# Optimization experiments

Hardware: AMD Instinct MI355X
Metric: run time of the kernel (lower is better)

Reference implementation:

```python
import jax, jax.numpy as jnp
import numpy as np

B = 4096          # fused tokens (batch)
E = 1024          # attnConfig embed_size == MoE emb_size
OUT = E // 4      # per-branch feature dim (self.output)
N_EXP = 8         # number of experts
TOP = 2           # top-k routing
H = 8             # attention heads
HD = E // H       # head dim
HID = 4 * E       # expert MLP hidden
IMG = 64 * 64     # flattened single-channel image
W_IMP = 0.01      # importance loss weight


def setup_inputs() -> dict:
    key = jax.random.key(0)
    ks = jax.random.split(key, 24)
    n = lambda i, shp, sc=1.0: jax.random.normal(ks[i], shp, jnp.float32) * sc
    inp = {
        'source': n(0, (B, 1, 64, 64)),
        'target': n(1, (B, 1, 64, 64)),
        'background': n(2, (B, 1, 64, 64)),
        'image': n(3, (B, E)),
        'text': n(4, (B, E)),
        # shared encoder (stub: flatten -> fc to OUT, shared across s/t/b)
        'W_enc': n(5, (IMG, OUT), 0.02), 'b_enc': jnp.zeros((OUT,), jnp.float32),
        # linerImg
        'W_img': n(6, (E, OUT), 0.02), 'b_img': jnp.zeros((OUT,), jnp.float32),
        # cross attention
        'Wq': n(7, (E, E), 0.02), 'bq': jnp.zeros((E,), jnp.float32),
        'Wk': n(8, (E, E), 0.02), 'bk': jnp.zeros((E,), jnp.float32),
        'Wv': n(9, (E, E), 0.02), 'bv': jnp.zeros((E,), jnp.float32),
        'Wo': n(10, (E, E), 0.02), 'bo': jnp.zeros((E,), jnp.float32),
        # gate
        'W_gate': n(11, (E, N_EXP), 0.02), 'b_gate': jnp.zeros((N_EXP,), jnp.float32),
        # experts: per-expert 2-layer MLP E->HID->E
        'W1': n(12, (N_EXP, E, HID), 0.02), 'b1': jnp.zeros((N_EXP, HID), jnp.float32),
        'W2': n(13, (N_EXP, HID, E), 0.02), 'b2': jnp.zeros((N_EXP, E), jnp.float32),
    }
    return inp


def reference(source, target, background, image, text,
              W_enc, b_enc, W_img, b_img,
              Wq, bq, Wk, bk, Wv, bv, Wo, bo,
              W_gate, b_gate, W1, b1, W2, b2):
    enc = lambda a: a.reshape(a.shape[0], -1) @ W_enc + b_enc      # shared_encoder stub
    s = enc(source); t = enc(target); bg = enc(background)        # [B, OUT] each
    img = jax.nn.silu(image @ W_img + b_img)                      # [B, OUT]
    x = jnp.concatenate([s, t, bg, img], axis=1)                  # [B, E] visionFeatures

    # cross attention with seq_len 1 for both x (query) and text (key/value)
    q = (x @ Wq + bq).reshape(B, H, HD)
    k = (text @ Wk + bk).reshape(B, H, HD)
    v = (text @ Wv + bv).reshape(B, H, HD)
    scores = jnp.sum(q * k, axis=-1, keepdims=True) / jnp.sqrt(jnp.float32(HD))  # [B,H,1]
    attw = jax.nn.softmax(scores[..., None], axis=-1)[..., 0]     # softmax over 1 key == 1
    att = (attw * v).reshape(B, E) @ Wo + bo                       # [B, E]

    gate_logits = att @ W_gate + b_gate                            # [B, N_EXP]
    gate_prob = jax.nn.softmax(gate_logits, axis=-1)               # eval mode: no noise
    top_w, top_idx = jax.lax.top_k(gate_prob, TOP)                 # [B, TOP]
    top_w = jax.nn.softmax(top_w, axis=-1)                         # renormalize over top-k

    # dense-dispatch equivalent of the per-expert gather/index_add loop
    h = jax.nn.gelu(jnp.einsum('be,neh->nbh', x, W1) + b1[:, None, :])   # [N,B,HID]
    y_all = jnp.einsum('nbh,nhe->nbe', h, W2) + b2[:, None, :]           # [N,B,E]
    combine = jnp.zeros((B, N_EXP), jnp.float32).at[
        jnp.arange(B)[:, None], top_idx].add(top_w)                      # [B,N]
    y = jnp.einsum('nbe,bn->be', y_all, combine)                          # [B,E]

    importance = gate_prob.sum(axis=0)                             # [N_EXP]
    importance_loss = W_IMP * (jnp.std(importance, ddof=1) / jnp.mean(importance)) ** 2
    return (y, gate_prob, importance_loss)
```

## Files before the change

kernel.cpp:

```cpp
#include <hip/hip_runtime.h>
#include <hip/hip_bf16.h>
#include <stdint.h>

typedef __bf16 bf16_t;
typedef bf16_t bf16x8 __attribute__((ext_vector_type(8)));
typedef float f32x4 __attribute__((ext_vector_type(4)));
typedef uint16_t u16x8 __attribute__((ext_vector_type(8)));

static constexpr int B_TOK  = 4096;
static constexpr int E_DIM  = 1024;
static constexpr int N_EXPC = 8;
static constexpr int HID    = 4096;
static constexpr int IMGSZ  = 4096;
static constexpr int NSLOT  = 2 * B_TOK;
static constexpr int NTIL   = 71;

#define DEVI __device__ __forceinline__

DEVI int imin(int a, int b) { return a < b ? a : b; }

DEVI uint16_t f2bf(float f) {
  union { float f; uint32_t u; } v; v.f = f;
  uint32_t u = v.u;
  return (uint16_t)((u + 0x7FFFu + ((u >> 16) & 1u)) >> 16);
}

DEVI void gload_lds16(const void* g, void* l) {
  __builtin_amdgcn_global_load_lds((const __attribute__((address_space(1))) void*)g,
                                   (__attribute__((address_space(3))) void*)l, 16, 0, 0);
}

template<int N> DEVI void waitv() {
  if constexpr (N == 0)       asm volatile("s_waitcnt vmcnt(0)" ::: "memory");
  else if constexpr (N == 4)  asm volatile("s_waitcnt vmcnt(4)" ::: "memory");
  else if constexpr (N == 8)  asm volatile("s_waitcnt vmcnt(8)" ::: "memory");
  else if constexpr (N == 10) asm volatile("s_waitcnt vmcnt(10)" ::: "memory");
}

#define BAR() do { __builtin_amdgcn_sched_barrier(0); __builtin_amdgcn_s_barrier(); \
                   __builtin_amdgcn_sched_barrier(0); } while (0)

#define MFMA16(a, b, c) __builtin_amdgcn_mfma_f32_16x16x32_bf16((a), (b), (c), 0, 0, 0)

DEVI void transW_body(int bid, const float* W1, const float* W2,
                      const float* We, const float* Wi,
                      uint16_t* W1T, uint16_t* W2T, uint16_t* WeT, uint16_t* WiT,
                      float (*tile)[65])
{
  const float* in; uint16_t* out; int R, C, c0, r0;
  if (bid < 8192) {
    int e = bid >> 10, rem = bid & 1023;
    R = 1024; C = 4096;
    c0 = (rem & 63) * 64; r0 = (rem >> 6) * 64;
    in = W1 + (size_t)e * R * C; out = W1T + (size_t)e * R * C;
  } else if (bid < 16384) {
    int i = bid - 8192; int e = i >> 10, rem = i & 1023;
    R = 4096; C = 1024;
    c0 = (rem & 15) * 64; r0 = (rem >> 4) * 64;
    in = W2 + (size_t)e * R * C; out = W2T + (size_t)e * R * C;
  } else if (bid < 16640) {
    int i = bid - 16384;
    R = 4096; C = 256;
    c0 = (i & 3) * 64; r0 = (i >> 2) * 64;
    in = We; out = WeT;
  } else {
    int i = bid - 16640;
    R = 1024; C = 256;
    c0 = (i & 3) * 64; r0 = (i >> 2) * 64;
    in = Wi; out = WiT;
  }
  int t = threadIdx.x;
  #pragma unroll
  for (int i = 0; i < 4; ++i) {
    int rr = i * 16 + (t >> 4), c4 = (t & 15) * 4;
    f32x4 v = *(const f32x4*)&in[(size_t)(r0 + rr) * C + c0 + c4];
    tile[rr][c4 + 0] = v[0]; tile[rr][c4 + 1] = v[1];
    tile[rr][c4 + 2] = v[2]; tile[rr][c4 + 3] = v[3];
  }
  __syncthreads();
  #pragma unroll
  for (int i = 0; i < 2; ++i) {
    int c = i * 32 + (t >> 3), j = t & 7;
    u16x8 o;
    #pragma unroll
    for (int k = 0; k < 8; ++k) o[k] = f2bf(tile[j * 8 + k][c]);
    *(u16x8*)&out[(size_t)(c0 + c) * R + r0 + j * 8] = o;
  }
}

DEVI void matf_body(int kblk, const float* W, const float* G, float* out)
{
  int k = kblk * 4 + (threadIdx.x >> 6);
  int lane = threadIdx.x & 63;
  float a0 = 0.f, a1 = 0.f, a2 = 0.f, a3 = 0.f, a4 = 0.f, a5 = 0.f, a6 = 0.f, a7 = 0.f;
  for (int m = lane; m < E_DIM; m += 64) {
    float w = W[(size_t)k * E_DIM + m];
    const float* gm = &G[m * 8];
    a0 = __builtin_fmaf(w, gm[0], a0); a1 = __builtin_fmaf(w, gm[1], a1);
    a2 = __builtin_fmaf(w, gm[2], a2); a3 = __builtin_fmaf(w, gm[3], a3);
    a4 = __builtin_fmaf(w, gm[4], a4); a5 = __builtin_fmaf(w, gm[5], a5);
    a6 = __builtin_fmaf(w, gm[6], a6); a7 = __builtin_fmaf(w, gm[7], a7);
  }
  #pragma unroll
  for (int off = 32; off; off >>= 1) {
    a0 += __shfl_xor(a0, off); a1 += __shfl_xor(a1, off);
    a2 += __shfl_xor(a2, off); a3 += __shfl_xor(a3, off);
    a4 += __shfl_xor(a4, off); a5 += __shfl_xor(a5, off);
    a6 += __shfl_xor(a6, off); a7 += __shfl_xor(a7, off);
  }
  if (lane == 0) {
    float* o = &out[k * 8];
    o[0] = a0; o[1] = a1; o[2] = a2; o[3] = a3;
    o[4] = a4; o[5] = a5; o[6] = a6; o[7] = a7;
  }
}

__global__ __launch_bounds__(256)
void prep1_k(const float* __restrict__ W1, const float* __restrict__ W2,
             const float* __restrict__ We, const float* __restrict__ Wi,
             uint16_t* __restrict__ W1T, uint16_t* __restrict__ W2T,
             uint16_t* __restrict__ WeT, uint16_t* __restrict__ WiT,
             const float* __restrict__ Wo, const float* __restrict__ Wg,
             float* __restrict__ g1c,
             const float* __restrict__ bv, float* __restrict__ part,
             int* __restrict__ counts)
{
  __shared__ float tile[64][65];
  int bid = blockIdx.x;
  if (bid < 16704) {
    transW_body(bid, W1, W2, We, Wi, W1T, W2T, WeT, WiT, tile);
  } else if (bid < 16960) {
    matf_body(bid - 16704, Wo, Wg, g1c);
  } else if (bid < 16968) {
    int b = bid - 16960, t = threadIdx.x;
    f32x4 acc = {0.f, 0.f, 0.f, 0.f};
    for (int k = b * 128; k < b * 128 + 128; ++k) {
      float s = bv[k];
      f32x4 w = *(const f32x4*)&Wo[(size_t)k * E_DIM + t * 4];
      acc[0] = __builtin_fmaf(s, w[0], acc[0]);
      acc[1] = __builtin_fmaf(s, w[1], acc[1]);
      acc[2] = __builtin_fmaf(s, w[2], acc[2]);
      acc[3] = __builtin_fmaf(s, w[3], acc[3]);
    }
    *(f32x4*)&part[(size_t)b * E_DIM + t * 4] = acc;
  } else {
    if (threadIdx.x < 8) counts[threadIdx.x] = 0;
  }
}

__global__ __launch_bounds__(256)
void prep2_k(const float* __restrict__ Wv, const float* __restrict__ g1c,
             float* __restrict__ G3,
             const float* __restrict__ part, const float* __restrict__ bo,
             const float* __restrict__ Wg, const float* __restrict__ bg,
             float* __restrict__ gb)
{
  int bid = blockIdx.x;
  if (bid < 256) {
    matf_body(bid, Wv, g1c, G3);
  } else {
    __shared__ float t1s[E_DIM];
    int t = threadIdx.x;
    for (int j = t; j < E_DIM; j += 256) {
      float s = bo[j];
      #pragma unroll
      for (int b = 0; b < 8; ++b) s += part[(size_t)b * E_DIM + j];
      t1s[j] = s;
    }
    __syncthreads();
    int wave = t >> 6, lane = t & 63;
    #pragma unroll
    for (int ei = 0; ei < 2; ++ei) {
      int e = wave * 2 + ei;
      float s = 0.f;
      for (int m = lane; m < E_DIM; m += 64) s = __builtin_fmaf(t1s[m], Wg[m * 8 + e], s);
      #pragma unroll
      for (int off = 32; off; off >>= 1) s += __shfl_xor(s, off);
      if (lane == 0) gb[e] = s + bg[e];
    }
  }
}

__global__ __launch_bounds__(256)
void gate_k(const float* __restrict__ text, const float* __restrict__ G3,
            const float* __restrict__ gb, float* __restrict__ gate_out,
            int* __restrict__ topIdx, float* __restrict__ topW,
            int* __restrict__ counts)
{
  __shared__ __align__(16) float sT[E_DIM];
  __shared__ float lg[8];
  int b = blockIdx.x, t = threadIdx.x;
  *(f32x4*)&sT[t * 4] = *(const f32x4*)&text[(size_t)b * E_DIM + t * 4];
  __syncthreads();
  int wave = t >> 6, lane = t & 63;
  #pragma unroll
  for (int ei = 0; ei < 2; ++ei) {
    int e = wave * 2 + ei;
    float s = 0.f;
    for (int k = lane; k < E_DIM; k += 64) s = __builtin_fmaf(sT[k], G3[k * 8 + e], s);
    #pragma unroll
    for (int off = 32; off; off >>= 1) s += __shfl_down(s, off);
    if (lane == 0) lg[e] = s + gb[e];
  }
  __syncthreads();
  if (t == 0) {
    float p[8];
    float mx = lg[0];
    for (int i = 1; i < 8; i++) mx = fmaxf(mx, lg[i]);
    float den = 0.f;
    for (int i = 0; i < 8; i++) { p[i] = __expf(lg[i] - mx); den += p[i]; }
    float inv = 1.f / den;
    for (int i = 0; i < 8; i++) { p[i] *= inv; gate_out[(size_t)b * 8 + i] = p[i]; }
    int i1 = 0;
    for (int i = 1; i < 8; i++) if (p[i] > p[i1]) i1 = i;
    int i2 = (i1 == 0) ? 1 : 0;
    for (int i = 0; i < 8; i++) if (i != i1 && p[i] > p[i2]) i2 = i;
    float ex = __expf(p[i2] - p[i1]);
    float w1 = 1.f / (1.f + ex), w2 = ex / (1.f + ex);
    topIdx[b * 2] = i1; topIdx[b * 2 + 1] = i2;
    topW[b * 2] = w1;  topW[b * 2 + 1] = w2;
    atomicAdd(&counts[i1], 1);
    atomicAdd(&counts[i2], 1);
  }
}

__global__ __launch_bounds__(256)
void post_k(const float* __restrict__ gate_out, float* __restrict__ out_loss,
            const int* __restrict__ counts, const int* __restrict__ topIdx,
            const float* __restrict__ topW,
            int* __restrict__ meta, int* __restrict__ perm,
            int* __restrict__ slotOf)
{
  int t = threadIdx.x;
  if (blockIdx.x == 0) {
    float s[8] = {0.f, 0.f, 0.f, 0.f, 0.f, 0.f, 0.f, 0.f};
    for (int b = t; b < B_TOK; b += 256) {
      const float* g = &gate_out[(size_t)b * 8];
      #pragma unroll
      for (int e = 0; e < 8; ++e) s[e] += g[e];
    }
    __shared__ float red[8][256];
    #pragma unroll
    for (int e = 0; e < 8; ++e) red[e][t] = s[e];
    __syncthreads();
    for (int off = 128; off; off >>= 1) {
      if (t < off)
        #pragma unroll
        for (int e = 0; e < 8; ++e) red[e][t] += red[e][t + off];
      __syncthreads();
    }
    if (t == 0) {
      float m = 0.f;
      for (int e = 0; e < 8; e++) m += red[e][0];
      m *= 0.125f;
      float v = 0.f;
      for (int e = 0; e < 8; e++) { float d = red[e][0] - m; v += d * d; }
      v /= 7.f;
      out_loss[0] = 0.01f * v / (m * m);
    }
  } else {
    __shared__ int sBases[8];
    __shared__ int sCursor[8];
    if (t == 0) {
      int a = 0, nt = 0;
      for (int e = 0; e < 8; e++) {
        sBases[e] = a; sCursor[e] = 0;
        int c = counts[e];
        for (int j = 0; j < c; j += 128) {
          meta[1 + 3 * nt] = e;
          meta[2 + 3 * nt] = a + j;
          meta[3 + 3 * nt] = (c - j < 128) ? (c - j) : 128;
          nt++;
        }
        a += c;
      }
      meta[0] = nt;
    }
    __syncthreads();
    for (int b = t; b < B_TOK; b += 256) {
      #pragma unroll
      for (int j = 0; j < 2; j++) {
        int e = topIdx[b * 2 + j];
        int pos = atomicAdd(&sCursor[e], 1);
        int slot = sBases[e] + pos;
        perm[slot] = b;
        slotOf[b * 2 + j] = slot;
      }
    }
  }
}

template<int BN, int EPI, bool GATHER, int NT>
__global__ __launch_bounds__(256, 3)
void gemm_p(const uint16_t* __restrict__ Ab, int lda,
            const uint16_t* __restrict__ BT, void* __restrict__ Cv, int ldc,
            const float* __restrict__ bias, int K,
            const int* __restrict__ meta, const int* __restrict__ perm,
            size_t bStride, int biasStride)
{
  constexpr int HN = BN / 2, FN = BN / 32;
  constexpr int OPS = (BN == 128 ? 4 : 3);
  constexpr int TOTAL = NTIL * NT, Q = TOTAL / 8, FULLB = 64 * NT;
  int bid = blockIdx.x;
  int wg = (bid & 7) * Q + (bid >> 3);
  int mtile, nt;
  if (wg < FULLB) { int rem = wg % (8 * NT); mtile = (wg / (8 * NT)) * 8 + (rem & 7); nt = rem >> 3; }
  else            { int rem = wg - FULLB;    mtile = 64 + rem % 7;                    nt = rem / 7; }
  if (mtile >= meta[0]) return;
  int e = meta[1 + 3 * mtile], rowBase = meta[2 + 3 * mtile], rows = meta[3 + 3 * mtile];
  const uint16_t* Bt = BT + (size_t)e * bStride;
  const float* bi = bias + (size_t)e * (size_t)biasStride;

  constexpr int ABUF = 8192;
  constexpr int BBUF = (BN == 128) ? 8192 : 4096;
  __shared__ __align__(16) char sAraw[3 * ABUF];
  __shared__ __align__(16) char sBraw[3 * BBUF];

  int t = threadIdx.x, wave = t >> 6, lane = t & 63;
  int wr = wave >> 1, wc = wave & 1;

  int rB = t >> 2;
  int slB = ((t & 3) ^ (rB & 3)) * 8;
  const uint16_t* gB0 = Bt + (size_t)(nt * BN + rB) * K + slB;
  const uint16_t* gB1 = Bt + (size_t)(nt * BN + rB + 64) * K + slB;

  int r0 = t >> 2, r1 = r0 + 64;
  int sl = ((t & 3) ^ (r0 & 3)) * 8;
  int rr0 = imin(r0, rows - 1), rr1 = imin(r1, rows - 1);
  int car0 = GATHER ? perm[rowBase + rr0] : rowBase + rr0;
  int car1 = GATHER ? perm[rowBase + rr1] : rowBase + rr1;
  const uint16_t* gA0 = Ab + (size_t)car0 * lda + sl;
  const uint16_t* gA1 = Ab + (size_t)car1 * lda + sl;

  char* laW = sAraw + wave * 1024;
  char* lbW = sBraw + wave * 1024;
  auto STAGE = [&](int kt, int c) {
    int ko = kt << 5;
    char* la = laW + c * ABUF;
    char* lb = lbW + c * BBUF;
    gload_lds16(gA0 + ko, la);
    gload_lds16(gA1 + ko, la + 4096);
    gload_lds16(gB0 + ko, lb);
    if constexpr (BN == 128) gload_lds16(gB1 + ko, lb + 4096);
  };

  f32x4 acc[4][FN];
  #pragma unroll
  for (int m = 0; m < 4; m++)
    #pragma unroll
    for (int n = 0; n < FN; n++)
      acc[m][n] = f32x4{0.f, 0.f, 0.f, 0.f};

  STAGE(0, 0);
  STAGE(1, 1);

  int fr = lane & 15;
  int rdoff = ((lane >> 4) ^ (lane & 3)) * 16;
  int c0 = 0, c2 = 2;
  int nk = K >> 5;

  for (int kt = 0; kt < nk; ++kt) {
    if (kt + 2 < nk) { STAGE(kt + 2, c2); waitv<2 * OPS>(); }
    else if (kt + 1 < nk) waitv<OPS>();
    else waitv<0>();
    BAR();

    const char* bA = sAraw + c0 * ABUF;
    const char* bB = sBraw + c0 * BBUF;
    bf16x8 af[4], bfr[FN];
    #pragma unroll
    for (int m = 0; m < 4; m++)
      af[m] = *(const bf16x8*)(bA + (wr * 64 + m * 16 + fr) * 64 + rdoff);
    #pragma unroll
    for (int n = 0; n < FN; n++)
      bfr[n] = *(const bf16x8*)(bB + (wc * HN + n * 16 + fr) * 64 + rdoff);
    #pragma unroll
    for (int m = 0; m < 4; m++)
      #pragma unroll
      for (int n = 0; n < FN; n++)
        acc[m][n] = MFMA16(af[m], bfr[n], acc[m][n]);

    BAR();
    c0 = (c0 == 2) ? 0 : c0 + 1;
    c2 = (c2 == 2) ? 0 : c2 + 1;
  }

  #pragma unroll
  for (int m = 0; m < 4; m++) {
    int lrow = wr * 64 + m * 16 + (lane >> 4) * 4;
    #pragma unroll
    for (int n = 0; n < FN; n++) {
      int col = nt * BN + wc * HN + n * 16 + (lane & 15);
      float bval = bi[col];
      #pragma unroll
      for (int r = 0; r < 4; r++) {
        int lr = lrow + r;
        if (lr >= rows) continue;
        float v = acc[m][n][r] + bval;
        size_t cr = (size_t)(rowBase + lr) * ldc + col;
        if (EPI == 3) {
          float u = v + 0.044715f * v * v * v;
          v = v / (1.f + __expf(-1.5957691216057308f * u));
          ((uint16_t*)Cv)[cr] = f2bf(v);
        } else {
          ((float*)Cv)[cr] = v;
        }
      }
    }
  }
}

__global__ __launch_bounds__(256, 3)
void gemm_encR(const float* __restrict__ F0, const float* __restrict__ F1,
               const float* __restrict__ F2, const float* __restrict__ Fimg,
               const uint16_t* __restrict__ BTe, const uint16_t* __restrict__ BTi,
               float* __restrict__ Penc, float* __restrict__ Pimg)
{
  int z = blockIdx.z;
  const float* Af; const uint16_t* BT; float* P; int K, kc;
  if (z < 12) {
    int br = z / 4; kc = z % 4;
    Af = (br == 0) ? F0 : (br == 1) ? F1 : F2;
    BT = BTe; P = Penc + (size_t)z * B_TOK * 256; K = IMGSZ;
  } else {
    kc = z - 12;
    Af = Fimg; BT = BTi; P = Pimg + (size_t)kc * B_TOK * 256; K = E_DIM;
  }
  int Kc = (z < 12) ? (K / 4) : (K / 2);
  int k0 = kc * Kc;
  int rowBase = blockIdx.x * 64, nt = blockIdx.y;

  __shared__ __align__(16) char sB[3 * 8192];
  int t = threadIdx.x, wave = t >> 6, lane = t & 63;
  int fr = lane & 15, q4 = lane >> 4;

  const float* gA = Af + (size_t)(rowBase + wave * 16 + fr) * K + k0 + q4 * 8;

  int rloc = t >> 2;
  int ssw = ((t & 3) ^ (rloc & 3)) * 8;
  const uint16_t* gB0 = BT + (size_t)(nt * 128 + rloc) * K + k0 + ssw;
  const uint16_t* gB1 = gB0 + (size_t)64 * K;

  auto STB = [&](int kt, int c) {
    gload_lds16(gB0 + kt * 32, sB + c * 8192 + wave * 1024);
    gload_lds16(gB1 + kt * 32, sB + c * 8192 + 4096 + wave * 1024);
  };

  f32x4 acc[8];
  #pragma unroll
  for (int n = 0; n < 8; ++n) acc[n] = f32x4{0.f, 0.f, 0.f, 0.f};

  int nk = Kc >> 5;
  STB(0, 0); STB(1, 1);
  f32x4 aE0 = *(const f32x4*)(gA),      aE1 = *(const f32x4*)(gA + 4);
  f32x4 aO0 = *(const f32x4*)(gA + 32), aO1 = *(const f32x4*)(gA + 36);
  int c0 = 0, c2 = 2;
  int bRow = (q4 ^ (fr & 3)) * 16;

  auto step = [&](int kt, f32x4& aX0, f32x4& aX1) {
    bool m2 = kt + 2 < nk;
    if (m2) STB(kt + 2, c2);
    bf16x8 a;
    a[0] = (bf16_t)aX0[0]; a[1] = (bf16_t)aX0[1]; a[2] = (bf16_t)aX0[2]; a[3] = (bf16_t)aX0[3];
    a[4] = (bf16_t)aX1[0]; a[5] = (bf16_t)aX1[1]; a[6] = (bf16_t)aX1[2]; a[7] = (bf16_t)aX1[3];
    int kp = m2 ? kt + 2 : kt;
    aX0 = *(const f32x4*)(gA + kp * 32);
    aX1 = *(const f32x4*)(gA + kp * 32 + 4);
    if (m2) waitv<10>(); else waitv<0>();
    BAR();
    const char* bb = sB + c0 * 8192;
    bf16x8 bfr[8];
    #pragma unroll
    for (int n = 0; n < 8; ++n)
      bfr[n] = *(const bf16x8*)(bb + n * 1024 + fr * 64 + bRow);
    #pragma unroll
    for (int n = 0; n < 8; ++n) acc[n] = MFMA16(a, bfr[n], acc[n]);
    BAR();
    c0 = (c0 == 2) ? 0 : c0 + 1;
    c2 = (c2 == 2) ? 0 : c2 + 1;
  };

  for (int kt = 0; kt < nk; kt += 2) {
    step(kt, aE0, aE1);
    step(kt + 1, aO0, aO1);
  }

  #pragma unroll
  for (int n = 0; n < 8; ++n) {
    int col = nt * 128 + n * 16 + fr;
    #pragma unroll
    for (int r = 0; r < 4; ++r) {
      int row = rowBase + wave * 16 + q4 * 4 + r;
      P[(size_t)row * 256 + col] = acc[n][r];
    }
  }
}

__global__ __launch_bounds__(256)
void redu_k(const float* __restrict__ Penc, const float* __restrict__ Pimg,
            const float* __restrict__ bEnc, const float* __restrict__ bImg,
            uint16_t* __restrict__ xb)
{
  int y = blockIdx.y;
  int row = blockIdx.x * 4 + (threadIdx.x >> 6);
  int c4 = (threadIdx.x & 63) * 4;
  bool img = (y == 3);
  const float* bias = img ? bImg : bEnc;
  f32x4 s = *(const f32x4*)&bias[c4];
  const float* p = (img ? Pimg : Penc + (size_t)y * 4 * B_TOK * 256)
                   + (size_t)row * 256 + c4;
  int SK = img ? 2 : 4;
  for (int kc = 0; kc < SK; ++kc)
    s += *(const f32x4*)(p + (size_t)kc * B_TOK * 256);
  if (img) {
    #pragma unroll
    for (int j = 0; j < 4; ++j) s[j] = s[j] / (1.f + __expf(-s[j]));
  }
  ushort4 o;
  o.x = f2bf(s[0]); o.y = f2bf(s[1]); o.z = f2bf(s[2]); o.w = f2bf(s[3]);
  *(ushort4*)&xb[(size_t)row * E_DIM + y * 256 + c4] = o;
}

__global__ __launch_bounds__(256)
void combine_k(const float* __restrict__ Yg, const int* __restrict__ slotOf,
               const float* __restrict__ topW, float* __restrict__ y)
{
  int b = blockIdx.x, t = threadIdx.x;
  int s0 = slotOf[b * 2], s1 = slotOf[b * 2 + 1];
  float w0 = topW[b * 2], w1 = topW[b * 2 + 1];
  f32x4 a = *(const f32x4*)&Yg[(size_t)s0 * E_DIM + t * 4];
  f32x4 c = *(const f32x4*)&Yg[(size_t)s1 * E_DIM + t * 4];
  f32x4 r = a * w0 + c * w1;
  *(f32x4*)&y[(size_t)b * E_DIM + t * 4] = r;
}

extern "C" void kernel_launch(void* const* d_in, const int* in_sizes, int n_in,
                              void* d_out, int out_size, void* d_ws, size_t ws_size,
                              hipStream_t stream)
{
  (void)in_sizes; (void)n_in; (void)out_size;
  const float* src   = (const float*)d_in[0];
  const float* tgt   = (const float*)d_in[1];
  const float* bgr   = (const float*)d_in[2];
  const float* image = (const float*)d_in[3];
  const float* text  = (const float*)d_in[4];
  const float* W_enc = (const float*)d_in[5];
  const float* b_enc = (const float*)d_in[6];
  const float* W_img = (const float*)d_in[7];
  const float* b_img = (const float*)d_in[8];
  const float* Wv    = (const float*)d_in[13];
  const float* bv    = (const float*)d_in[14];
  const float* Wo    = (const float*)d_in[15];
  const float* bo    = (const float*)d_in[16];
  const float* Wg    = (const float*)d_in[17];
  const float* bgg   = (const float*)d_in[18];
  const float* W1    = (const float*)d_in[19];
  const float* b1    = (const float*)d_in[20];
  const float* W2    = (const float*)d_in[21];
  const float* b2    = (const float*)d_in[22];

  float* out_y    = (float*)d_out;
  float* out_gate = out_y + (size_t)B_TOK * E_DIM;
  float* out_loss = out_gate + (size_t)B_TOK * N_EXPC;

  char* p = (char*)d_ws;
  auto alloc = [&](size_t bytes) { char* r = p; p += (bytes + 255) & ~(size_t)255; return r; };
  uint16_t* WencT = (uint16_t*)alloc((size_t)256 * IMGSZ * 2);
  uint16_t* WimgT = (uint16_t*)alloc((size_t)256 * E_DIM * 2);
  uint16_t* W1T   = (uint16_t*)alloc((size_t)N_EXPC * HID * E_DIM * 2);
  uint16_t* W2T   = (uint16_t*)alloc((size_t)N_EXPC * E_DIM * HID * 2);
  float* part  = (float*)alloc((size_t)8 * E_DIM * 4);
  float* g1c   = (float*)alloc((size_t)E_DIM * 8 * 4);
  float* G3    = (float*)alloc((size_t)E_DIM * 8 * 4);
  float* gbv   = (float*)alloc(64 * 4);
  int*   topIdx = (int*)alloc(B_TOK * 2 * 4);
  float* topW   = (float*)alloc(B_TOK * 2 * 4);
  int*   slotOf = (int*)alloc(B_TOK * 2 * 4);
  int*   counts = (int*)alloc(64 * 4);
  int*   meta   = (int*)alloc((1 + 3 * (NTIL + 1)) * 4 + 64);
  int*   perm   = (int*)alloc(NSLOT * 4);
  uint16_t* xbf  = (uint16_t*)alloc((size_t)B_TOK * E_DIM * 2);
  uint16_t* Hbuf = (uint16_t*)alloc((size_t)NSLOT * HID * 2);
  char* uni = alloc((size_t)14 * B_TOK * 256 * 4);
  float* Penc = (float*)uni;
  float* Pimg = Penc + (size_t)12 * B_TOK * 256;
  float* Yg   = (float*)uni;
  if ((size_t)(p - (char*)d_ws) > ws_size) return;

  prep1_k<<<dim3(16969), 256, 0, stream>>>(W1, W2, W_enc, W_img, W1T, W2T, WencT, WimgT,
                                           Wo, Wg, g1c, bv, part, counts);
  prep2_k<<<dim3(257), 256, 0, stream>>>(Wv, g1c, G3, part, bo, Wg, bgg, gbv);
  gate_k<<<B_TOK, 256, 0, stream>>>(text, G3, gbv, out_gate, topIdx, topW, counts);
  post_k<<<dim3(2), 256, 0, stream>>>(out_gate, out_loss, counts, topIdx, topW,
                                      meta, perm, slotOf);
  gemm_encR<<<dim3(B_TOK / 64, 2, 14), 256, 0, stream>>>(
      src, tgt, bgr, image, WencT, WimgT, Penc, Pimg);
  redu_k<<<dim3(B_TOK / 4, 4), 256, 0, stream>>>(Penc, Pimg, b_enc, b_img, xbf);

  gemm_p<128, 3, true, HID / 128><<<dim3(NTIL * (HID / 128)), 256, 0, stream>>>(
      xbf, E_DIM, W1T, Hbuf, HID, b1, E_DIM, meta, perm, (size_t)HID * E_DIM, HID);
  gemm_p<128, 0, false, E_DIM / 128><<<dim3(NTIL * (E_DIM / 128)), 256, 0, stream>>>(
      Hbuf, HID, W2T, Yg, E_DIM, b2, HID, meta, perm, (size_t)E_DIM * HID, E_DIM);

  combine_k<<<B_TOK, 256, 0, stream>>>(Yg, slotOf, topW, out_y);
}
```

Before: 636.6 us.

## Halve encoder split-K, fuse routing into reduction kernel, store expert output in bf16

The encoder GEMM now splits K in two instead of four (the image branch is not split at all), which halves the partial-sum buffers written and read by the reduction. The routing/post kernel is merged into the reduction kernel as extra blocks, removing one launch. The second expert GEMM writes bf16 instead of fp32, and the combine kernel converts it back, cutting the traffic for the expert output. The trade-offs are fewer encoder blocks, hence less parallelism, and an extra bf16 rounding of the expert outputs before they are combined.

```diff
diff --git a/kernel.cpp b/kernel.cpp
--- a/kernel.cpp
+++ b/kernel.cpp
@@ -23,6 +23,10 @@
   union { float f; uint32_t u; } v; v.f = f;
   uint32_t u = v.u;
   return (uint16_t)((u + 0x7FFFu + ((u >> 16) & 1u)) >> 16);
+}
+
+DEVI float bf2f(uint16_t u) {
+  union { uint32_t i; float f; } v; v.i = (uint32_t)u << 16; return v.f;
 }
 
 DEVI void gload_lds16(const void* g, void* l) {
@@ -224,14 +228,244 @@
   }
 }
 
+template<int BN, int EPI, bool GATHER, int NT>
+__global__ __launch_bounds__(256, 3)
+void gemm_p(const uint16_t* __restrict__ Ab, int lda,
+            const uint16_t* __restrict__ BT, void* __restrict__ Cv, int ldc,
+            const float* __restrict__ bias, int K,
+            const int* __restrict__ meta, const int* __restrict__ perm,
+            size_t bStride, int biasStride)
+{
+  constexpr int HN = BN / 2, FN = BN / 32;
+  constexpr int OPS = (BN == 128 ? 4 : 3);
+  constexpr int TOTAL = NTIL * NT, Q = TOTAL / 8, FULLB = 64 * NT;
+  int bid = blockIdx.x;
+  int wg = (bid & 7) * Q + (bid >> 3);
+  int mtile, nt;
+  if (wg < FULLB) { int rem = wg % (8 * NT); mtile = (wg / (8 * NT)) * 8 + (rem & 7); nt = rem >> 3; }
+  else            { int rem = wg - FULLB;    mtile = 64 + rem % 7;                    nt = rem / 7; }
+  if (mtile >= meta[0]) return;
+  int e = meta[1 + 3 * mtile], rowBase = meta[2 + 3 * mtile], rows = meta[3 + 3 * mtile];
+  const uint16_t* Bt = BT + (size_t)e * bStride;
+  const float* bi = bias + (size_t)e * (size_t)biasStride;
+
+  constexpr int ABUF = 8192;
+  constexpr int BBUF = (BN == 128) ? 8192 : 4096;
+  __shared__ __align__(16) char sAraw[3 * ABUF];
+  __shared__ __align__(16) char sBraw[3 * BBUF];
+
+  int t = threadIdx.x, wave = t >> 6, lane = t & 63;
+  int wr = wave >> 1, wc = wave & 1;
+
+  int rB = t >> 2;
+  int slB = ((t & 3) ^ (rB & 3)) * 8;
+  const uint16_t* gB0 = Bt + (size_t)(nt * BN + rB) * K + slB;
+  const uint16_t* gB1 = Bt + (size_t)(nt * BN + rB + 64) * K + slB;
+
+  int r0 = t >> 2, r1 = r0 + 64;
+  int sl = ((t & 3) ^ (r0 & 3)) * 8;
+  int rr0 = imin(r0, rows - 1), rr1 = imin(r1, rows - 1);
+  int car0 = GATHER ? perm[rowBase + rr0] : rowBase + rr0;
+  int car1 = GATHER ? perm[rowBase + rr1] : rowBase + rr1;
+  const uint16_t* gA0 = Ab + (size_t)car0 * lda + sl;
+  const uint16_t* gA1 = Ab + (size_t)car1 * lda + sl;
+
+  char* laW = sAraw + wave * 1024;
+  char* lbW = sBraw + wave * 1024;
+  auto STAGE = [&](int kt, int c) {
+    int ko = kt << 5;
+    char* la = laW + c * ABUF;
+    char* lb = lbW + c * BBUF;
+    gload_lds16(gA0 + ko, la);
+    gload_lds16(gA1 + ko, la + 4096);
+    gload_lds16(gB0 + ko, lb);
+    if constexpr (BN == 128) gload_lds16(gB1 + ko, lb + 4096);
+  };
+
+  f32x4 acc[4][FN];
+  #pragma unroll
+  for (int m = 0; m < 4; m++)
+    #pragma unroll
+    for (int n = 0; n < FN; n++)
+      acc[m][n] = f32x4{0.f, 0.f, 0.f, 0.f};
+
+  STAGE(0, 0);
+  STAGE(1, 1);
+
+  int fr = lane & 15;
+  int rdoff = ((lane >> 4) ^ (lane & 3)) * 16;
+  int c0 = 0, c2 = 2;
+  int nk = K >> 5;
+
+  for (int kt = 0; kt < nk; ++kt) {
+    if (kt + 2 < nk) { STAGE(kt + 2, c2); waitv<2 * OPS>(); }
+    else if (kt + 1 < nk) waitv<OPS>();
+    else waitv<0>();
+    BAR();
+
+    const char* bA = sAraw + c0 * ABUF;
+    const char* bB = sBraw + c0 * BBUF;
+    bf16x8 af[4], bfr[FN];
+    #pragma unroll
+    for (int m = 0; m < 4; m++)
+      af[m] = *(const bf16x8*)(bA + (wr * 64 + m * 16 + fr) * 64 + rdoff);
+    #pragma unroll
+    for (int n = 0; n < FN; n++)
+      bfr[n] = *(const bf16x8*)(bB + (wc * HN + n * 16 + fr) * 64 + rdoff);
+    #pragma unroll
+    for (int m = 0; m < 4; m++)
+      #pragma unroll
+      for (int n = 0; n < FN; n++)
+        acc[m][n] = MFMA16(af[m], bfr[n], acc[m][n]);
+
+    BAR();
+    c0 = (c0 == 2) ? 0 : c0 + 1;
+    c2 = (c2 == 2) ? 0 : c2 + 1;
+  }
+
+  #pragma unroll
+  for (int m = 0; m < 4; m++) {
+    int lrow = wr * 64 + m * 16 + (lane >> 4) * 4;
+    #pragma unroll
+    for (int n = 0; n < FN; n++) {
+      int col = nt * BN + wc * HN + n * 16 + (lane & 15);
+      float bval = bi[col];
+      #pragma unroll
+      for (int r = 0; r < 4; r++) {
+        int lr = lrow + r;
+        if (lr >= rows) continue;
+        float v = acc[m][n][r] + bval;
+        size_t cr = (size_t)(rowBase + lr) * ldc + col;
+        if (EPI == 3) {
+          float u = v + 0.044715f * v * v * v;
+          v = v / (1.f + __expf(-1.5957691216057308f * u));
+          ((uint16_t*)Cv)[cr] = f2bf(v);
+        } else if (EPI == 1) {
+          ((uint16_t*)Cv)[cr] = f2bf(v);
+        } else {
+          ((float*)Cv)[cr] = v;
+        }
+      }
+    }
+  }
+}
+
+__global__ __launch_bounds__(256, 3)
+void gemm_encR(const float* __restrict__ F0, const float* __restrict__ F1,
+               const float* __restrict__ F2, const float* __restrict__ Fimg,
+               const uint16_t* __restrict__ BTe, const uint16_t* __restrict__ BTi,
+               float* __restrict__ Penc, float* __restrict__ Pimg)
+{
+  int z = blockIdx.z;
+  const float* Af; const uint16_t* BT; float* P; int K, Kc, k0;
+  if (z < 6) {
+    int br = z >> 1, kc = z & 1;
+    Af = (br == 0) ? F0 : (br == 1) ? F1 : F2;
+    BT = BTe; P = Penc + (size_t)z * B_TOK * 256;
+    K = IMGSZ; Kc = IMGSZ / 2; k0 = kc * Kc;
+  } else {
+    Af = Fimg; BT = BTi; P = Pimg;
+    K = E_DIM; Kc = E_DIM; k0 = 0;
+  }
+  int rowBase = blockIdx.x * 64, nt = blockIdx.y;
+
+  __shared__ __align__(16) char sB[3 * 8192];
+  int t = threadIdx.x, wave = t >> 6, lane = t & 63;
+  int fr = lane & 15, q4 = lane >> 4;
+
+  const float* gA = Af + (size_t)(rowBase + wave * 16 + fr) * K + k0 + q4 * 8;
+
+  int rloc = t >> 2;
+  int ssw = ((t & 3) ^ (rloc & 3)) * 8;
+  const uint16_t* gB0 = BT + (size_t)(nt * 128 + rloc) * K + k0 + ssw;
+  const uint16_t* gB1 = gB0 + (size_t)64 * K;
+
+  auto STB = [&](int kt, int c) {
+    gload_lds16(gB0 + kt * 32, sB + c * 8192 + wave * 1024);
+    gload_lds16(gB1 + kt * 32, sB + c * 8192 + 4096 + wave * 1024);
+  };
+
+  f32x4 acc[8];
+  #pragma unroll
+  for (int n = 0; n < 8; ++n) acc[n] = f32x4{0.f, 0.f, 0.f, 0.f};
+
+  int nk = Kc >> 5;
+  STB(0, 0); STB(1, 1);
+  f32x4 aE0 = *(const f32x4*)(gA),      aE1 = *(const f32x4*)(gA + 4);
+  f32x4 aO0 = *(const f32x4*)(gA + 32), aO1 = *(const f32x4*)(gA + 36);
+  int c0 = 0, c2 = 2;
+  int bRow = (q4 ^ (fr & 3)) * 16;
+
+  auto step = [&](int kt, f32x4& aX0, f32x4& aX1) {
+    bool m2 = kt + 2 < nk;
+    if (m2) STB(kt + 2, c2);
+    bf16x8 a;
+    a[0] = (bf16_t)aX0[0]; a[1] = (bf16_t)aX0[1]; a[2] = (bf16_t)aX0[2]; a[3] = (bf16_t)aX0[3];
+    a[4] = (bf16_t)aX1[0]; a[5] = (bf16_t)aX1[1]; a[6] = (bf16_t)aX1[2]; a[7] = (bf16_t)aX1[3];
+    int kp = m2 ? kt + 2 : kt;
+    aX0 = *(const f32x4*)(gA + kp * 32);
+    aX1 = *(const f32x4*)(gA + kp * 32 + 4);
+    if (m2) waitv<10>(); else waitv<0>();
+    BAR();
+    const char* bb = sB + c0 * 8192;
+    bf16x8 bfr[8];
+    #pragma unroll
+    for (int n = 0; n < 8; ++n)
+      bfr[n] = *(const bf16x8*)(bb + n * 1024 + fr * 64 + bRow);
+    #pragma unroll
+    for (int n = 0; n < 8; ++n) acc[n] = MFMA16(a, bfr[n], acc[n]);
+    BAR();
+    c0 = (c0 == 2) ? 0 : c0 + 1;
+    c2 = (c2 == 2) ? 0 : c2 + 1;
+  };
+
+  for (int kt = 0; kt < nk; kt += 2) {
+    step(kt, aE0, aE1);
+    step(kt + 1, aO0, aO1);
+  }
+
+  #pragma unroll
+  for (int n = 0; n < 8; ++n) {
+    int col = nt * 128 + n * 16 + fr;
+    #pragma unroll
+    for (int r = 0; r < 4; ++r) {
+      int row = rowBase + wave * 16 + q4 * 4 + r;
+      P[(size_t)row * 256 + col] = acc[n][r];
+    }
+  }
+}
+
 __global__ __launch_bounds__(256)
-void post_k(const float* __restrict__ gate_out, float* __restrict__ out_loss,
-            const int* __restrict__ counts, const int* __restrict__ topIdx,
-            const float* __restrict__ topW,
-            int* __restrict__ meta, int* __restrict__ perm,
-            int* __restrict__ slotOf)
-{
-  int t = threadIdx.x;
+void redupost_k(const float* __restrict__ Penc, const float* __restrict__ Pimg,
+                const float* __restrict__ bEnc, const float* __restrict__ bImg,
+                uint16_t* __restrict__ xb,
+                const float* __restrict__ gate_out, float* __restrict__ out_loss,
+                const int* __restrict__ counts, const int* __restrict__ topIdx,
+                const float* __restrict__ topW,
+                int* __restrict__ meta, int* __restrict__ perm,
+                int* __restrict__ slotOf)
+{
+  int y = blockIdx.y, t = threadIdx.x;
+  if (y < 4) {
+    int row = blockIdx.x * 4 + (t >> 6);
+    int c4 = (t & 63) * 4;
+    bool img = (y == 3);
+    const float* bias = img ? bImg : bEnc;
+    f32x4 s = *(const f32x4*)&bias[c4];
+    if (img) {
+      s += *(const f32x4*)&Pimg[(size_t)row * 256 + c4];
+      #pragma unroll
+      for (int j = 0; j < 4; ++j) s[j] = s[j] / (1.f + __expf(-s[j]));
+    } else {
+      const float* p = Penc + (size_t)y * 2 * B_TOK * 256 + (size_t)row * 256 + c4;
+      s += *(const f32x4*)p;
+      s += *(const f32x4*)(p + (size_t)B_TOK * 256);
+    }
+    ushort4 o;
+    o.x = f2bf(s[0]); o.y = f2bf(s[1]); o.z = f2bf(s[2]); o.w = f2bf(s[3]);
+    *(ushort4*)&xb[(size_t)row * E_DIM + y * 256 + c4] = o;
+    return;
+  }
   if (blockIdx.x == 0) {
     float s[8] = {0.f, 0.f, 0.f, 0.f, 0.f, 0.f, 0.f, 0.f};
     for (int b = t; b < B_TOK; b += 256) {
@@ -258,7 +492,7 @@
       v /= 7.f;
       out_loss[0] = 0.01f * v / (m * m);
     }
-  } else {
+  } else if (blockIdx.x == 1) {
     __shared__ int sBases[8];
     __shared__ int sCursor[8];
     if (t == 0) {
@@ -290,247 +524,20 @@
   }
 }
 
-template<int BN, int EPI, bool GATHER, int NT>
-__global__ __launch_bounds__(256, 3)
-void gemm_p(const uint16_t* __restrict__ Ab, int lda,
-            const uint16_t* __restrict__ BT, void* __restrict__ Cv, int ldc,
-            const float* __restrict__ bias, int K,
-            const int* __restrict__ meta, const int* __restrict__ perm,
-            size_t bStride, int biasStride)
-{
-  constexpr int HN = BN / 2, FN = BN / 32;
-  constexpr int OPS = (BN == 128 ? 4 : 3);
-  constexpr int TOTAL = NTIL * NT, Q = TOTAL / 8, FULLB = 64 * NT;
-  int bid = blockIdx.x;
-  int wg = (bid & 7) * Q + (bid >> 3);
-  int mtile, nt;
-  if (wg < FULLB) { int rem = wg % (8 * NT); mtile = (wg / (8 * NT)) * 8 + (rem & 7); nt = rem >> 3; }
-  else            { int rem = wg - FULLB;    mtile = 64 + rem % 7;                    nt = rem / 7; }
-  if (mtile >= meta[0]) return;
-  int e = meta[1 + 3 * mtile], rowBase = meta[2 + 3 * mtile], rows = meta[3 + 3 * mtile];
-  const uint16_t* Bt = BT + (size_t)e * bStride;
-  const float* bi = bias + (size_t)e * (size_t)biasStride;
-
-  constexpr int ABUF = 8192;
-  constexpr int BBUF = (BN == 128) ? 8192 : 4096;
-  __shared__ __align__(16) char sAraw[3 * ABUF];
-  __shared__ __align__(16) char sBraw[3 * BBUF];
-
-  int t = threadIdx.x, wave = t >> 6, lane = t & 63;
-  int wr = wave >> 1, wc = wave & 1;
-
-  int rB = t >> 2;
-  int slB = ((t & 3) ^ (rB & 3)) * 8;
-  const uint16_t* gB0 = Bt + (size_t)(nt * BN + rB) * K + slB;
-  const uint16_t* gB1 = Bt + (size_t)(nt * BN + rB + 64) * K + slB;
-
-  int r0 = t >> 2, r1 = r0 + 64;
-  int sl = ((t & 3) ^ (r0 & 3)) * 8;
-  int rr0 = imin(r0, rows - 1), rr1 = imin(r1, rows - 1);
-  int car0 = GATHER ? perm[rowBase + rr0] : rowBase + rr0;
-  int car1 = GATHER ? perm[rowBase + rr1] : rowBase + rr1;
-  const uint16_t* gA0 = Ab + (size_t)car0 * lda + sl;
-  const uint16_t* gA1 = Ab + (size_t)car1 * lda + sl;
-
-  char* laW = sAraw + wave * 1024;
-  char* lbW = sBraw + wave * 1024;
-  auto STAGE = [&](int kt, int c) {
-    int ko = kt << 5;
-    char* la = laW + c * ABUF;
-    char* lb = lbW + c * BBUF;
-    gload_lds16(gA0 + ko, la);
-    gload_lds16(gA1 + ko, la + 4096);
-    gload_lds16(gB0 + ko, lb);
-    if constexpr (BN == 128) gload_lds16(gB1 + ko, lb + 4096);
-  };
-
-  f32x4 acc[4][FN];
-  #pragma unroll
-  for (int m = 0; m < 4; m++)
-    #pragma unroll
-    for (int n = 0; n < FN; n++)
-      acc[m][n] = f32x4{0.f, 0.f, 0.f, 0.f};
-
-  STAGE(0, 0);
-  STAGE(1, 1);
-
-  int fr = lane & 15;
-  int rdoff = ((lane >> 4) ^ (lane & 3)) * 16;
-  int c0 = 0, c2 = 2;
-  int nk = K >> 5;
-
-  for (int kt = 0; kt < nk; ++kt) {
-    if (kt + 2 < nk) { STAGE(kt + 2, c2); waitv<2 * OPS>(); }
-    else if (kt + 1 < nk) waitv<OPS>();
-    else waitv<0>();
-    BAR();
-
-    const char* bA = sAraw + c0 * ABUF;
-    const char* bB = sBraw + c0 * BBUF;
-    bf16x8 af[4], bfr[FN];
-    #pragma unroll
-    for (int m = 0; m < 4; m++)
-      af[m] = *(const bf16x8*)(bA + (wr * 64 + m * 16 + fr) * 64 + rdoff);
-    #pragma unroll
-    for (int n = 0; n < FN; n++)
-      bfr[n] = *(const bf16x8*)(bB + (wc * HN + n * 16 + fr) * 64 + rdoff);
-    #pragma unroll
-    for (int m = 0; m < 4; m++)
-      #pragma unroll
-      for (int n = 0; n < FN; n++)
-        acc[m][n] = MFMA16(af[m], bfr[n], acc[m][n]);
-
-    BAR();
-    c0 = (c0 == 2) ? 0 : c0 + 1;
-    c2 = (c2 == 2) ? 0 : c2 + 1;
-  }
-
-  #pragma unroll
-  for (int m = 0; m < 4; m++) {
-    int lrow = wr * 64 + m * 16 + (lane >> 4) * 4;
-    #pragma unroll
-    for (int n = 0; n < FN; n++) {
-      int col = nt * BN + wc * HN + n * 16 + (lane & 15);
-      float bval = bi[col];
-      #pragma unroll
-      for (int r = 0; r < 4; r++) {
-        int lr = lrow + r;
-        if (lr >= rows) continue;
-        float v = acc[m][n][r] + bval;
-        size_t cr = (size_t)(rowBase + lr) * ldc + col;
-        if (EPI == 3) {
-          float u = v + 0.044715f * v * v * v;
-          v = v / (1.f + __expf(-1.5957691216057308f * u));
-          ((uint16_t*)Cv)[cr] = f2bf(v);
-        } else {
-          ((float*)Cv)[cr] = v;
-        }
-      }
-    }
-  }
-}
-
-__global__ __launch_bounds__(256, 3)
-void gemm_encR(const float* __restrict__ F0, const float* __restrict__ F1,
-               const float* __restrict__ F2, const float* __restrict__ Fimg,
-               const uint16_t* __restrict__ BTe, const uint16_t* __restrict__ BTi,
-               float* __restrict__ Penc, float* __restrict__ Pimg)
-{
-  int z = blockIdx.z;
-  const float* Af; const uint16_t* BT; float* P; int K, kc;
-  if (z < 12) {
-    int br = z / 4; kc = z % 4;
-    Af = (br == 0) ? F0 : (br == 1) ? F1 : F2;
-    BT = BTe; P = Penc + (size_t)z * B_TOK * 256; K = IMGSZ;
-  } else {
-    kc = z - 12;
-    Af = Fimg; BT = BTi; P = Pimg + (size_t)kc * B_TOK * 256; K = E_DIM;
-  }
-  int Kc = (z < 12) ? (K / 4) : (K / 2);
-  int k0 = kc * Kc;
-  int rowBase = blockIdx.x * 64, nt = blockIdx.y;
-
-  __shared__ __align__(16) char sB[3 * 8192];
-  int t = threadIdx.x, wave = t >> 6, lane = t & 63;
-  int fr = lane & 15, q4 = lane >> 4;
-
-  const float* gA = Af + (size_t)(rowBase + wave * 16 + fr) * K + k0 + q4 * 8;
-
-  int rloc = t >> 2;
-  int ssw = ((t & 3) ^ (rloc & 3)) * 8;
-  const uint16_t* gB0 = BT + (size_t)(nt * 128 + rloc) * K + k0 + ssw;
-  const uint16_t* gB1 = gB0 + (size_t)64 * K;
-
-  auto STB = [&](int kt, int c) {
-    gload_lds16(gB0 + kt * 32, sB + c * 8192 + wave * 1024);
-    gload_lds16(gB1 + kt * 32, sB + c * 8192 + 4096 + wave * 1024);
-  };
-
-  f32x4 acc[8];
-  #pragma unroll
-  for (int n = 0; n < 8; ++n) acc[n] = f32x4{0.f, 0.f, 0.f, 0.f};
-
-  int nk = Kc >> 5;
-  STB(0, 0); STB(1, 1);
-  f32x4 aE0 = *(const f32x4*)(gA),      aE1 = *(const f32x4*)(gA + 4);
-  f32x4 aO0 = *(const f32x4*)(gA + 32), aO1 = *(const f32x4*)(gA + 36);
-  int c0 = 0, c2 = 2;
-  int bRow = (q4 ^ (fr & 3)) * 16;
-
-  auto step = [&](int kt, f32x4& aX0, f32x4& aX1) {
-    bool m2 = kt + 2 < nk;
-    if (m2) STB(kt + 2, c2);
-    bf16x8 a;
-    a[0] = (bf16_t)aX0[0]; a[1] = (bf16_t)aX0[1]; a[2] = (bf16_t)aX0[2]; a[3] = (bf16_t)aX0[3];
-    a[4] = (bf16_t)aX1[0]; a[5] = (bf16_t)aX1[1]; a[6] = (bf16_t)aX1[2]; a[7] = (bf16_t)aX1[3];
-    int kp = m2 ? kt + 2 : kt;
-    aX0 = *(const f32x4*)(gA + kp * 32);
-    aX1 = *(const f32x4*)(gA + kp * 32 + 4);
-    if (m2) waitv<10>(); else waitv<0>();
-    BAR();
-    const char* bb = sB + c0 * 8192;
-    bf16x8 bfr[8];
-    #pragma unroll
-    for (int n = 0; n < 8; ++n)
-      bfr[n] = *(const bf16x8*)(bb + n * 1024 + fr * 64 + bRow);
-    #pragma unroll
-    for (int n = 0; n < 8; ++n) acc[n] = MFMA16(a, bfr[n], acc[n]);
-    BAR();
-    c0 = (c0 == 2) ? 0 : c0 + 1;
-    c2 = (c2 == 2) ? 0 : c2 + 1;
-  };
-
-  for (int kt = 0; kt < nk; kt += 2) {
-    step(kt, aE0, aE1);
-    step(kt + 1, aO0, aO1);
-  }
-
-  #pragma unroll
-  for (int n = 0; n < 8; ++n) {
-    int col = nt * 128 + n * 16 + fr;
-    #pragma unroll
-    for (int r = 0; r < 4; ++r) {
-      int row = rowBase + wave * 16 + q4 * 4 + r;
-      P[(size_t)row * 256 + col] = acc[n][r];
-    }
-  }
-}
-
 __global__ __launch_bounds__(256)
-void redu_k(const float* __restrict__ Penc, const float* __restrict__ Pimg,
-            const float* __restrict__ bEnc, const float* __restrict__ bImg,
-            uint16_t* __restrict__ xb)
-{
-  int y = blockIdx.y;
-  int row = blockIdx.x * 4 + (threadIdx.x >> 6);
-  int c4 = (threadIdx.x & 63) * 4;
-  bool img = (y == 3);
-  const float* bias = img ? bImg : bEnc;
-  f32x4 s = *(const f32x4*)&bias[c4];
-  const float* p = (img ? Pimg : Penc + (size_t)y * 4 * B_TOK * 256)
-                   + (size_t)row * 256 + c4;
-  int SK = img ? 2 : 4;
-  for (int kc = 0; kc < SK; ++kc)
-    s += *(const f32x4*)(p + (size_t)kc * B_TOK * 256);
-  if (img) {
-    #pragma unroll
-    for (int j = 0; j < 4; ++j) s[j] = s[j] / (1.f + __expf(-s[j]));
-  }
-  ushort4 o;
-  o.x = f2bf(s[0]); o.y = f2bf(s[1]); o.z = f2bf(s[2]); o.w = f2bf(s[3]);
-  *(ushort4*)&xb[(size_t)row * E_DIM + y * 256 + c4] = o;
-}
-
-__global__ __launch_bounds__(256)
-void combine_k(const float* __restrict__ Yg, const int* __restrict__ slotOf,
+void combine_k(const uint16_t* __restrict__ Yg, const int* __restrict__ slotOf,
                const float* __restrict__ topW, float* __restrict__ y)
 {
   int b = blockIdx.x, t = threadIdx.x;
   int s0 = slotOf[b * 2], s1 = slotOf[b * 2 + 1];
   float w0 = topW[b * 2], w1 = topW[b * 2 + 1];
-  f32x4 a = *(const f32x4*)&Yg[(size_t)s0 * E_DIM + t * 4];
-  f32x4 c = *(const f32x4*)&Yg[(size_t)s1 * E_DIM + t * 4];
-  f32x4 r = a * w0 + c * w1;
+  ushort4 ua = *(const ushort4*)&Yg[(size_t)s0 * E_DIM + t * 4];
+  ushort4 uc = *(const ushort4*)&Yg[(size_t)s1 * E_DIM + t * 4];
+  f32x4 r;
+  r[0] = bf2f(ua.x) * w0 + bf2f(uc.x) * w1;
+  r[1] = bf2f(ua.y) * w0 + bf2f(uc.y) * w1;
+  r[2] = bf2f(ua.z) * w0 + bf2f(uc.z) * w1;
+  r[3] = bf2f(ua.w) * w0 + bf2f(uc.w) * w1;
   *(f32x4*)&y[(size_t)b * E_DIM + t * 4] = r;
 }
 
@@ -581,25 +588,25 @@
   int*   perm   = (int*)alloc(NSLOT * 4);
   uint16_t* xbf  = (uint16_t*)alloc((size_t)B_TOK * E_DIM * 2);
   uint16_t* Hbuf = (uint16_t*)alloc((size_t)NSLOT * HID * 2);
-  char* uni = alloc((size_t)14 * B_TOK * 256 * 4);
+  char* uni = alloc((size_t)7 * B_TOK * 256 * 4);
   float* Penc = (float*)uni;
-  float* Pimg = Penc + (size_t)12 * B_TOK * 256;
-  float* Yg   = (float*)uni;
+  float* Pimg = Penc + (size_t)6 * B_TOK * 256;
+  uint16_t* Yg = (uint16_t*)uni;
   if ((size_t)(p - (char*)d_ws) > ws_size) return;
 
   prep1_k<<<dim3(16969), 256, 0, stream>>>(W1, W2, W_enc, W_img, W1T, W2T, WencT, WimgT,
                                            Wo, Wg, g1c, bv, part, counts);
   prep2_k<<<dim3(257), 256, 0, stream>>>(Wv, g1c, G3, part, bo, Wg, bgg, gbv);
   gate_k<<<B_TOK, 256, 0, stream>>>(text, G3, gbv, out_gate, topIdx, topW, counts);
-  post_k<<<dim3(2), 256, 0, stream>>>(out_gate, out_loss, counts, topIdx, topW,
-                                      meta, perm, slotOf);
-  gemm_encR<<<dim3(B_TOK / 64, 2, 14), 256, 0, stream>>>(
+  gemm_encR<<<dim3(B_TOK / 64, 2, 7), 256, 0, stream>>>(
       src, tgt, bgr, image, WencT, WimgT, Penc, Pimg);
-  redu_k<<<dim3(B_TOK / 4, 4), 256, 0, stream>>>(Penc, Pimg, b_enc, b_img, xbf);
+  redupost_k<<<dim3(B_TOK / 4, 5), 256, 0, stream>>>(
+      Penc, Pimg, b_enc, b_img, xbf,
+      out_gate, out_loss, counts, topIdx, topW, meta, perm, slotOf);
 
   gemm_p<128, 3, true, HID / 128><<<dim3(NTIL * (HID / 128)), 256, 0, stream>>>(
       xbf, E_DIM, W1T, Hbuf, HID, b1, E_DIM, meta, perm, (size_t)HID * E_DIM, HID);
-  gemm_p<128, 0, false, E_DIM / 128><<<dim3(NTIL * (E_DIM / 128)), 256, 0, stream>>>(
+  gemm_p<128, 1, false, E_DIM / 128><<<dim3(NTIL * (E_DIM / 128)), 256, 0, stream>>>(
       Hbuf, HID, W2T, Yg, E_DIM, b2, HID, meta, perm, (size_t)E_DIM * HID, E_DIM);
 
   combine_k<<<B_TOK, 256, 0, stream>>>(Yg, slotOf, topW, out_y);
```

New measurement: 633.9 us (median of 2 runs). No clear change (-0.4%).
